# Optimization experiments

Measured on AMD Instinct MI355X. Metric: run time of the kernel, lower is better.

The kernel has to match this reference:

```python
import jax, jax.numpy as jnp
import numpy as np

# Grid derived from voxel_size=[0.2,0.2,0.2], pcr=[0,-40,-3,70.4,40,1]
NX, NY, NZ, NB = 352, 400, 20, 4


def setup_inputs() -> dict:
    key = jax.random.key(0)
    N, C = 1_000_000, 64
    kp, kb, kz, ky, kx = jax.random.split(key, 5)
    points = jax.random.normal(kp, (N, C), dtype=jnp.float32)
    b = jax.random.randint(kb, (N,), 0, NB)
    z = jax.random.randint(kz, (N,), 0, NZ)
    y = jax.random.randint(ky, (N,), 0, NY)
    x = jax.random.randint(kx, (N,), 0, NX)
    coors = jnp.stack([b, z, y, x], axis=1).astype(jnp.int32)
    return {"points": points, "coors": coors}


def reference(points, coors):
    # Dynamic scatter with mean reduction (average_points=True):
    # group points sharing the same (batch, z, y, x) voxel coordinate and
    # average their features. Padded (unused) voxel slots have coor == -1
    # and zero features, so the output shape is static ([N, C]).
    N = points.shape[0]
    b, z, y, x = coors[:, 0], coors[:, 1], coors[:, 2], coors[:, 3]
    keys = ((b.astype(jnp.int64) * NZ + z) * NY + y) * NX + x  # linearized voxel id

    uniq, inv = jnp.unique(keys, return_inverse=True, size=N, fill_value=-1)
    inv = inv.reshape(-1)

    sums = jax.ops.segment_sum(points, inv, num_segments=N)          # [N, C]
    counts = jax.ops.segment_sum(jnp.ones((N,), points.dtype), inv, num_segments=N)
    voxels = sums / jnp.maximum(counts, 1.0)[:, None]

    # decode linearized keys back to (batch, z, y, x); -1 marks padding
    valid = uniq >= 0
    ux = uniq % NX
    uy = (uniq // NX) % NY
    uz = (uniq // (NX * NY)) % NZ
    ub = uniq // (NX * NY * NZ)
    voxel_coors = jnp.stack([ub, uz, uy, ux], axis=1).astype(jnp.int32)
    voxel_coors = jnp.where(valid[:, None], voxel_coors, -1)
    return voxels, voxel_coors
```

## Files before the change

kernel.cpp:

```cpp
#include <hip/hip_runtime.h>
#include <stdint.h>

#define NXc 352
#define NYc 400
#define NZc 20
#define KS  11264000
#define WORDS 176000
#define NBLKS 688
#define NCH 64
#define RPT 8

#define OFF_A     0ull
#define OFF_P     11264000ull
#define OFF_R     12672000ull
#define OFF_DESC  13376000ull
#define OFF_NU    13381504ull
#define OFF_KEYPT 13381760ull
#define OFF_IOFF  17381760ull
#define OFF_PID   21381760ull

static __device__ __forceinline__ int keyof(int4 c) {
  return ((c.x * NZc + c.y) * NYc + c.z) * NXc + c.w;
}

static __device__ __forceinline__ unsigned long long packd(unsigned int st, unsigned int p, unsigned int c) {
  return ((unsigned long long)st << 62) | ((unsigned long long)p << 31) | (unsigned long long)c;
}

__global__ void k_zero(uint4* __restrict__ A4, unsigned int mA,
                       uint4* __restrict__ D4, unsigned int mD,
                       float4* __restrict__ C4, unsigned int mC) {
  unsigned int i = blockIdx.x * 256 + threadIdx.x, s = gridDim.x * 256;
  uint4 z = make_uint4(0u, 0u, 0u, 0u);
  for (unsigned int j = i; j < mA; j += s) A4[j] = z;
  for (unsigned int j = i; j < mD; j += s) D4[j] = z;
  float4 m1 = make_float4(-1.f, -1.f, -1.f, -1.f);
  for (unsigned int j = i; j < mC; j += s) C4[j] = m1;
}

__global__ void k_count(const int4* __restrict__ coors, unsigned int* __restrict__ A32,
                        int* __restrict__ keyPt, int n) {
  int p = blockIdx.x * 256 + threadIdx.x;
  if (p >= n) return;
  int key = keyof(coors[p]);
  keyPt[p] = key;
  atomicAdd(&A32[key >> 2], 1u << (8 * (key & 3)));
}

__global__ void k_scan(const unsigned char* __restrict__ A,
                       unsigned long long* __restrict__ desc,
                       unsigned long long* __restrict__ P, unsigned int* __restrict__ R,
                       unsigned int* __restrict__ ioff, unsigned int* __restrict__ nu,
                       float4* __restrict__ outc, int n) {
  int b = blockIdx.x, t = threadIdx.x;
  int w = b * 256 + t;
  unsigned long long mask = 0ull;
  unsigned int uu[16];
  unsigned int pres = 0, cnt = 0;
  if (w < WORDS) {
    const uint4* aw = (const uint4*)(A + (size_t)w * 64);
#pragma unroll
    for (int q = 0; q < 4; q++) {
      uint4 v = aw[q];
      uu[q * 4 + 0] = v.x; uu[q * 4 + 1] = v.y; uu[q * 4 + 2] = v.z; uu[q * 4 + 3] = v.w;
    }
#pragma unroll
    for (int i = 0; i < 16; i++) {
      unsigned int u = uu[i];
#pragma unroll
      for (int bb = 0; bb < 4; bb++) {
        unsigned int byte = (u >> (8 * bb)) & 0xFFu;
        cnt += byte;
        if (byte) mask |= 1ull << (i * 4 + bb);
      }
    }
    pres = (unsigned int)__popcll(mask);
  }
  __shared__ unsigned int sp[256], sc[256];
  sp[t] = pres; sc[t] = cnt; __syncthreads();
  unsigned int ip = pres, ic = cnt;
  for (int o = 1; o < 256; o <<= 1) {
    unsigned int ap = (t >= o) ? sp[t - o] : 0u;
    unsigned int ac = (t >= o) ? sc[t - o] : 0u;
    __syncthreads();
    ip += ap; ic += ac;
    sp[t] = ip; sc[t] = ic; __syncthreads();
  }
  __shared__ unsigned int exc2[2];
  if (t == 0) {
    unsigned int aggP = sp[255], aggC = sc[255];
    unsigned int eP = 0, eC = 0;
    if (b == 0) {
      atomicExch(&desc[0], packd(2u, aggP, aggC));
    } else {
      atomicExch(&desc[b], packd(1u, aggP, aggC));
      int j = b - 1;
      for (;;) {
        unsigned long long d = atomicAdd(&desc[j], 0ull);
        unsigned int st = (unsigned int)(d >> 62);
        if (st == 0u) continue;
        eP += (unsigned int)((d >> 31) & 0x7FFFFFFFull);
        eC += (unsigned int)(d & 0x7FFFFFFFull);
        if (st == 2u) break;
        --j;
      }
      atomicExch(&desc[b], packd(2u, eP + aggP, eC + aggC));
    }
    exc2[0] = eP; exc2[1] = eC;
    if (b == NBLKS - 1) {
      unsigned int tot = eP + aggP;
      nu[0] = tot;
      ioff[tot] = (unsigned int)n;
    }
  }
  __syncthreads();
  unsigned int excP = exc2[0], excC = exc2[1];
  if (w < WORDS) {
    unsigned int rank = excP + ip - pres;
    unsigned int coff = excC + ic - cnt;
    P[w] = mask; R[w] = rank;
    for (int j = 0; j < 64; j++) {
      unsigned int byte = (uu[j >> 2] >> (8 * (j & 3))) & 0xFFu;
      if (byte) {
        ioff[rank] = coff;
        unsigned int k = (unsigned int)w * 64u + (unsigned int)j;
        unsigned int x = k % NXc; unsigned int k2 = k / NXc;
        unsigned int y = k2 % NYc; unsigned int k3 = k2 / NYc;
        unsigned int z = k3 % NZc; unsigned int bb = k3 / NZc;
        outc[rank] = make_float4((float)bb, (float)z, (float)y, (float)x);
        rank++; coff += byte;
      }
    }
  }
}

__global__ void k_scatter(const int* __restrict__ keyPt, unsigned int* __restrict__ A32,
                          const unsigned long long* __restrict__ P, const unsigned int* __restrict__ R,
                          const unsigned int* __restrict__ ioff, unsigned int* __restrict__ pid, int n) {
  int p = blockIdx.x * 256 + threadIdx.x;
  if (p >= n) return;
  int key = keyPt[p];
  int w = key >> 6, bit = key & 63;
  unsigned int rank = R[w] + (unsigned int)__popcll(P[w] & ((1ull << bit) - 1ull));
  unsigned int sh = 8u * (unsigned int)(key & 3);
  unsigned int old = atomicSub(&A32[key >> 2], 1u << sh);
  unsigned int intra = ((old >> sh) & 0xFFu) - 1u;
  pid[ioff[rank] + intra] = (unsigned int)p;
}

__global__ void k_gather(const float4* __restrict__ pts, const unsigned int* __restrict__ pid,
                         const unsigned int* __restrict__ ioff, const unsigned int* __restrict__ nu,
                         float* __restrict__ out, int n) {
  int gt = blockIdx.x * 256 + threadIdx.x;
  int grp = gt >> 4, l = gt & 15;
  int rb = grp * RPT;
  if (rb >= n) return;
  unsigned int nU = nu[0];

  unsigned int e[RPT + 1];
#pragma unroll
  for (int j = 0; j <= RPT; j++) {
    unsigned int idx = min((unsigned int)(rb + j), nU);
    e[j] = ioff[idx];
  }

  unsigned int p0[RPT];
#pragma unroll
  for (int j = 0; j < RPT; j++)
    p0[j] = (e[j] < e[j + 1]) ? pid[e[j]] : 0u;

  float4 acc[RPT];
#pragma unroll
  for (int j = 0; j < RPT; j++) {
    if (e[j] < e[j + 1]) acc[j] = pts[(size_t)p0[j] * 16 + l];
    else                 acc[j] = make_float4(0.f, 0.f, 0.f, 0.f);
  }

#pragma unroll
  for (int j = 0; j < RPT; j++) {
    unsigned int span = e[j + 1] - e[j];
    for (unsigned int i = e[j] + 1; i < e[j + 1]; i++) {
      unsigned int p = pid[i];
      float4 v = pts[(size_t)p * 16 + l];
      acc[j].x += v.x; acc[j].y += v.y; acc[j].z += v.z; acc[j].w += v.w;
    }
    if (span > 1) {
      float inv = 1.0f / (float)span;
      acc[j].x *= inv; acc[j].y *= inv; acc[j].z *= inv; acc[j].w *= inv;
    }
  }

#pragma unroll
  for (int j = 0; j < RPT; j++) {
    int r = rb + j;
    if (r < n) ((float4*)out)[(size_t)r * 16 + l] = acc[j];
  }
}

extern "C" void kernel_launch(void* const* d_in, const int* in_sizes, int n_in,
                              void* d_out, int out_size, void* d_ws, size_t ws_size,
                              hipStream_t stream) {
  const float4* pts = (const float4*)d_in[0];
  const int4* coors = (const int4*)d_in[1];
  int n = in_sizes[1] / 4;
  float* out = (float*)d_out;
  char* ws = (char*)d_ws;
  unsigned char*      A    = (unsigned char*)(ws + OFF_A);
  unsigned int*       A32  = (unsigned int*)(ws + OFF_A);
  unsigned long long* P    = (unsigned long long*)(ws + OFF_P);
  unsigned int*       R    = (unsigned int*)(ws + OFF_R);
  unsigned long long* desc = (unsigned long long*)(ws + OFF_DESC);
  unsigned int*       nu   = (unsigned int*)(ws + OFF_NU);
  int*                keyPt= (int*)(ws + OFF_KEYPT);
  unsigned int*       ioff = (unsigned int*)(ws + OFF_IOFF);
  unsigned int*       pid  = (unsigned int*)(ws + OFF_PID);
  float4*             outc = (float4*)(out + (size_t)n * NCH);

  k_zero   <<<2048,  256, 0, stream>>>((uint4*)A, (unsigned int)(KS / 16),
                                       (uint4*)desc, (unsigned int)(NBLKS * 8 / 16),
                                       outc, (unsigned int)n);
  int nb = (n + 255) / 256;
  k_count  <<<nb,    256, 0, stream>>>(coors, A32, keyPt, n);
  k_scan   <<<NBLKS, 256, 0, stream>>>(A, desc, P, R, ioff, nu, outc, n);
  k_scatter<<<nb,    256, 0, stream>>>(keyPt, A32, P, R, ioff, pid, n);
  int ngrp = (n + RPT - 1) / RPT;
  int gb = (ngrp * 16 + 255) / 256;
  k_gather <<<gb,    256, 0, stream>>>(pts, pid, ioff, nu, out, n);
}
```

Baseline: 237.6 us.

## Write singleton voxels directly in scatter and gather only multi-point voxels

```diff
diff --git a/kernel.cpp b/kernel.cpp
--- a/kernel.cpp
+++ b/kernel.cpp
@@ -8,7 +8,6 @@
 #define WORDS 176000
 #define NBLKS 688
 #define NCH 64
-#define RPT 8
 
 #define OFF_A     0ull
 #define OFF_P     11264000ull
@@ -17,7 +16,8 @@
 #define OFF_NU    13381504ull
 #define OFF_KEYPT 13381760ull
 #define OFF_IOFF  17381760ull
-#define OFF_PID   21381760ull
+#define OFF_ML    21382016ull
+#define OFF_PID   23382016ull
 
 static __device__ __forceinline__ int keyof(int4 c) {
   return ((c.x * NZc + c.y) * NYc + c.z) * NXc + c.w;
@@ -28,14 +28,11 @@
 }
 
 __global__ void k_zero(uint4* __restrict__ A4, unsigned int mA,
-                       uint4* __restrict__ D4, unsigned int mD,
-                       float4* __restrict__ C4, unsigned int mC) {
+                       uint4* __restrict__ D4, unsigned int mD) {
   unsigned int i = blockIdx.x * 256 + threadIdx.x, s = gridDim.x * 256;
   uint4 z = make_uint4(0u, 0u, 0u, 0u);
   for (unsigned int j = i; j < mA; j += s) A4[j] = z;
   for (unsigned int j = i; j < mD; j += s) D4[j] = z;
-  float4 m1 = make_float4(-1.f, -1.f, -1.f, -1.f);
-  for (unsigned int j = i; j < mC; j += s) C4[j] = m1;
 }
 
 __global__ void k_count(const int4* __restrict__ coors, unsigned int* __restrict__ A32,
@@ -51,7 +48,7 @@
                        unsigned long long* __restrict__ desc,
                        unsigned long long* __restrict__ P, unsigned int* __restrict__ R,
                        unsigned int* __restrict__ ioff, unsigned int* __restrict__ nu,
-                       float4* __restrict__ outc, int n) {
+                       unsigned int* __restrict__ mlist, float4* __restrict__ outc, int n) {
   int b = blockIdx.x, t = threadIdx.x;
   int w = b * 256 + t;
   unsigned long long mask = 0ull;
@@ -128,73 +125,62 @@
         unsigned int y = k2 % NYc; unsigned int k3 = k2 / NYc;
         unsigned int z = k3 % NZc; unsigned int bb = k3 / NZc;
         outc[rank] = make_float4((float)bb, (float)z, (float)y, (float)x);
+        if (byte >= 2u) mlist[atomicAdd(&nu[1], 1u)] = rank;
         rank++; coff += byte;
       }
     }
   }
 }
 
-__global__ void k_scatter(const int* __restrict__ keyPt, unsigned int* __restrict__ A32,
+__global__ void k_scatter(const float4* __restrict__ pts, const int* __restrict__ keyPt,
+                          unsigned int* __restrict__ A32,
                           const unsigned long long* __restrict__ P, const unsigned int* __restrict__ R,
-                          const unsigned int* __restrict__ ioff, unsigned int* __restrict__ pid, int n) {
-  int p = blockIdx.x * 256 + threadIdx.x;
+                          const unsigned int* __restrict__ ioff, unsigned int* __restrict__ pid,
+                          float* __restrict__ out, int n) {
+  int gt = blockIdx.x * 256 + threadIdx.x;
+  int p = gt >> 4, l = gt & 15;
   if (p >= n) return;
   int key = keyPt[p];
   int w = key >> 6, bit = key & 63;
   unsigned int rank = R[w] + (unsigned int)__popcll(P[w] & ((1ull << bit) - 1ull));
-  unsigned int sh = 8u * (unsigned int)(key & 3);
-  unsigned int old = atomicSub(&A32[key >> 2], 1u << sh);
-  unsigned int intra = ((old >> sh) & 0xFFu) - 1u;
-  pid[ioff[rank] + intra] = (unsigned int)p;
-}
-
-__global__ void k_gather(const float4* __restrict__ pts, const unsigned int* __restrict__ pid,
-                         const unsigned int* __restrict__ ioff, const unsigned int* __restrict__ nu,
-                         float* __restrict__ out, int n) {
+  unsigned int o0 = ioff[rank], o1 = ioff[rank + 1];
+  if (o1 - o0 == 1u) {
+    float4 v = pts[(size_t)p * 16 + l];
+    ((float4*)out)[(size_t)rank * 16 + l] = v;
+  } else if (l == 0) {
+    unsigned int sh = 8u * (unsigned int)(key & 3);
+    unsigned int old = atomicSub(&A32[key >> 2], 1u << sh);
+    unsigned int intra = ((old >> sh) & 0xFFu) - 1u;
+    pid[o0 + intra] = (unsigned int)p;
+  }
+}
+
+__global__ void k_mg(const float4* __restrict__ pts, const unsigned int* __restrict__ pid,
+                     const unsigned int* __restrict__ ioff, const unsigned int* __restrict__ mlist,
+                     const unsigned int* __restrict__ nu, float* __restrict__ out) {
   int gt = blockIdx.x * 256 + threadIdx.x;
-  int grp = gt >> 4, l = gt & 15;
-  int rb = grp * RPT;
-  if (rb >= n) return;
-  unsigned int nU = nu[0];
-
-  unsigned int e[RPT + 1];
-#pragma unroll
-  for (int j = 0; j <= RPT; j++) {
-    unsigned int idx = min((unsigned int)(rb + j), nU);
-    e[j] = ioff[idx];
-  }
-
-  unsigned int p0[RPT];
-#pragma unroll
-  for (int j = 0; j < RPT; j++)
-    p0[j] = (e[j] < e[j + 1]) ? pid[e[j]] : 0u;
-
-  float4 acc[RPT];
-#pragma unroll
-  for (int j = 0; j < RPT; j++) {
-    if (e[j] < e[j + 1]) acc[j] = pts[(size_t)p0[j] * 16 + l];
-    else                 acc[j] = make_float4(0.f, 0.f, 0.f, 0.f);
-  }
-
-#pragma unroll
-  for (int j = 0; j < RPT; j++) {
-    unsigned int span = e[j + 1] - e[j];
-    for (unsigned int i = e[j] + 1; i < e[j + 1]; i++) {
-      unsigned int p = pid[i];
-      float4 v = pts[(size_t)p * 16 + l];
-      acc[j].x += v.x; acc[j].y += v.y; acc[j].z += v.z; acc[j].w += v.w;
-    }
-    if (span > 1) {
-      float inv = 1.0f / (float)span;
-      acc[j].x *= inv; acc[j].y *= inv; acc[j].z *= inv; acc[j].w *= inv;
-    }
-  }
-
-#pragma unroll
-  for (int j = 0; j < RPT; j++) {
-    int r = rb + j;
-    if (r < n) ((float4*)out)[(size_t)r * 16 + l] = acc[j];
-  }
+  int g = gt >> 4, l = gt & 15;
+  if ((unsigned int)g >= nu[1]) return;
+  unsigned int rank = mlist[g];
+  unsigned int o0 = ioff[rank], o1 = ioff[rank + 1];
+  float4 acc = make_float4(0.f, 0.f, 0.f, 0.f);
+  for (unsigned int i = o0; i < o1; i++) {
+    float4 v = pts[(size_t)pid[i] * 16 + l];
+    acc.x += v.x; acc.y += v.y; acc.z += v.z; acc.w += v.w;
+  }
+  float inv = 1.0f / (float)(o1 - o0);
+  acc.x *= inv; acc.y *= inv; acc.z *= inv; acc.w *= inv;
+  ((float4*)out)[(size_t)rank * 16 + l] = acc;
+}
+
+__global__ void k_tail(const unsigned int* __restrict__ nu, float* __restrict__ out, int n) {
+  int gt = blockIdx.x * 256 + threadIdx.x;
+  int r = gt >> 4, l = gt & 15;
+  if (r >= n) return;
+  if ((unsigned int)r < nu[0]) return;
+  ((float4*)out)[(size_t)r * 16 + l] = make_float4(0.f, 0.f, 0.f, 0.f);
+  if (l == 0)
+    ((float4*)(out + (size_t)n * NCH))[r] = make_float4(-1.f, -1.f, -1.f, -1.f);
 }
 
 extern "C" void kernel_launch(void* const* d_in, const int* in_sizes, int n_in,
@@ -213,17 +199,18 @@
   unsigned int*       nu   = (unsigned int*)(ws + OFF_NU);
   int*                keyPt= (int*)(ws + OFF_KEYPT);
   unsigned int*       ioff = (unsigned int*)(ws + OFF_IOFF);
+  unsigned int*       mlist= (unsigned int*)(ws + OFF_ML);
   unsigned int*       pid  = (unsigned int*)(ws + OFF_PID);
   float4*             outc = (float4*)(out + (size_t)n * NCH);
 
   k_zero   <<<2048,  256, 0, stream>>>((uint4*)A, (unsigned int)(KS / 16),
-                                       (uint4*)desc, (unsigned int)(NBLKS * 8 / 16),
-                                       outc, (unsigned int)n);
+                                       (uint4*)desc, (unsigned int)((5504 + 256) / 16));
   int nb = (n + 255) / 256;
   k_count  <<<nb,    256, 0, stream>>>(coors, A32, keyPt, n);
-  k_scan   <<<NBLKS, 256, 0, stream>>>(A, desc, P, R, ioff, nu, outc, n);
-  k_scatter<<<nb,    256, 0, stream>>>(keyPt, A32, P, R, ioff, pid, n);
-  int ngrp = (n + RPT - 1) / RPT;
-  int gb = (ngrp * 16 + 255) / 256;
-  k_gather <<<gb,    256, 0, stream>>>(pts, pid, ioff, nu, out, n);
-}
+  k_scan   <<<NBLKS, 256, 0, stream>>>(A, desc, P, R, ioff, nu, mlist, outc, n);
+  int sb = (n * 16 + 255) / 256;
+  k_scatter<<<sb,    256, 0, stream>>>(pts, keyPt, A32, P, R, ioff, pid, out, n);
+  int mb = ((n / 2) * 16 + 255) / 256;
+  k_mg     <<<mb,    256, 0, stream>>>(pts, pid, ioff, mlist, nu, out);
+  k_tail   <<<sb,    256, 0, stream>>>(nu, out, n);
+}
```

Result: slower. 645.9 us (+171.8%).
